# Kernel tuning notes

Measured on AMD Instinct MI355X. Metric: run time of the kernel, lower is better.

The kernel has to match this reference:

```python
import jax, jax.numpy as jnp
import numpy as np

B = 2
C = 96
NH = 4
HD = C // NH
DEPTH = 2
LAT, LON = 181, 360
WH, WW = 6, 12
N = WH * WW
PT, PBm, PL, PR = 2, 3, 0, 0
H, W = LAT + PT + PBm, LON + PL + PR
SH, SW = WH // 2, WW // 2
NWH, NWW = H // WH, W // WW
NW = NWH * NWW
SCALE = HD ** -0.5

def _rel_index():
    ch, cw = np.meshgrid(np.arange(WH), np.arange(WW), indexing='ij')
    coords = np.stack([ch, cw]).reshape(2, -1)
    rel = (coords[:, :, None] - coords[:, None, :]).transpose(1, 2, 0).astype(np.int64)
    rel[:, :, 0] += WH - 1
    rel[:, :, 1] += WW - 1
    rel[:, :, 0] *= 2 * WW - 1
    return rel.sum(-1)  # (N, N)

REL_IDX = jnp.asarray(_rel_index())

def _shift_mask():
    img = np.zeros((H, W))
    cnt = 0
    for hs in (slice(0, -WH), slice(-WH, -SH), slice(-SH, None)):
        for ws in (slice(0, -WW), slice(-WW, -SW), slice(-SW, None)):
            img[hs, ws] = cnt
            cnt += 1
    mw = img.reshape(NWH, WH, NWW, WW).transpose(0, 2, 1, 3).reshape(NW, N)
    am = mw[:, None, :] - mw[:, :, None]
    return np.where(am != 0, -100.0, 0.0).astype(np.float32)

ATTN_MASK = jnp.asarray(_shift_mask())  # (NW, N, N)

def _ln(x, g, b):
    m = x.mean(-1, keepdims=True)
    v = x.var(-1, keepdims=True)
    return (x - m) * jax.lax.rsqrt(v + 1e-5) * g + b

def _win_part(x):
    b = x.shape[0]
    return x.reshape(b, NWH, WH, NWW, WW, C).transpose(0, 1, 3, 2, 4, 5).reshape(-1, N, C)

def _win_rev(xw, b):
    return xw.reshape(b, NWH, NWW, WH, WW, C).transpose(0, 1, 3, 2, 4, 5).reshape(b, H, W, C)

def _block(x, shift, g1, b1, qw, qb, pw, pb, rpb, g2, b2, f1w, f1b, f2w, f2b):
    b = x.shape[0]
    sc = x
    x = _ln(x, g1, b1)
    if shift:
        x = jnp.roll(x, (-SH, -SW), (1, 2))
    xw = _win_part(x)  # (b*NW, N, C)
    qkv = (xw @ qw.T + qb).reshape(-1, N, 3, NH, HD).transpose(2, 0, 3, 1, 4)
    q, k, v = qkv[0], qkv[1], qkv[2]  # each (b*NW, NH, N, HD)
    attn = (q * SCALE) @ k.transpose(0, 1, 3, 2)  # (b*NW, NH, N, N)
    bias = rpb[REL_IDX].transpose(2, 0, 1)  # (NH, N, N)
    attn = attn + bias[None]
    if shift:
        attn = (attn.reshape(b, NW, NH, N, N) + ATTN_MASK[None, :, None]).reshape(-1, NH, N, N)
    attn = jax.nn.softmax(attn, axis=-1)
    out = (attn @ v).transpose(0, 2, 1, 3).reshape(-1, N, C)
    out = out @ pw.T + pb
    x = _win_rev(out, b)
    if shift:
        x = jnp.roll(x, (SH, SW), (1, 2))
    x = sc + x
    h = _ln(x, g2, b2)
    h = jax.nn.gelu(h @ f1w.T + f1b) @ f2w.T + f2b
    return x + h

def _forward(x, g1, b1, qkv_w, qkv_b, proj_w, proj_b, rpb, g2, b2, fc1_w, fc1_b, fc2_w, fc2_b):
    x = jnp.pad(x, ((0, 0), (0, 0), (PT, PBm), (PL, PR)))  # ZeroPad2d
    x = x.transpose(0, 2, 3, 1)  # (B, H, W, C)
    for i in range(DEPTH):
        x = _block(x, i % 2 == 1, g1[i], b1[i], qkv_w[i], qkv_b[i], proj_w[i], proj_b[i],
                   rpb[i], g2[i], b2[i], fc1_w[i], fc1_b[i], fc2_w[i], fc2_b[i])
    x = x.transpose(0, 3, 1, 2)
    return x[:, :, PT:H - PBm, PL:W - PR]


def setup_inputs() -> dict:
    key = jax.random.key(0)
    ks = jax.random.split(key, 6)
    s = 0.02
    tbl = (2 * WH - 1) * (2 * WW - 1)
    return {
        'x': jax.random.normal(ks[0], (B, C, LAT, LON), jnp.float32),
        'g1': jnp.ones((DEPTH, C), jnp.float32),
        'b1': jnp.zeros((DEPTH, C), jnp.float32),
        'qkv_w': jax.random.normal(ks[1], (DEPTH, 3 * C, C), jnp.float32) * s,
        'qkv_b': jnp.zeros((DEPTH, 3 * C), jnp.float32),
        'proj_w': jax.random.normal(ks[2], (DEPTH, C, C), jnp.float32) * s,
        'proj_b': jnp.zeros((DEPTH, C), jnp.float32),
        'rpb': jax.random.normal(ks[3], (DEPTH, tbl, NH), jnp.float32) * s,
        'g2': jnp.ones((DEPTH, C), jnp.float32),
        'b2': jnp.zeros((DEPTH, C), jnp.float32),
        'fc1_w': jax.random.normal(ks[4], (DEPTH, 4 * C, C), jnp.float32) * s,
        'fc1_b': jnp.zeros((DEPTH, 4 * C), jnp.float32),
        'fc2_w': jax.random.normal(ks[5], (DEPTH, C, 4 * C), jnp.float32) * s,
        'fc2_b': jnp.zeros((DEPTH, C), jnp.float32),
    }


def reference(x, g1, b1, qkv_w, qkv_b, proj_w, proj_b, rpb, g2, b2, fc1_w, fc1_b, fc2_w, fc2_b):
    return _forward(x, g1, b1, qkv_w, qkv_b, proj_w, proj_b, rpb, g2, b2, fc1_w, fc1_b, fc2_w, fc2_b)
```

## Files before the change

kernel.cpp:

```cpp
#include <hip/hip_runtime.h>
#include <math.h>

#define BB    2
#define CC    96
#define NHD   4
#define HDIM  24
#define LAT_  181
#define LON_  360
#define PT_   2
#define HH    186
#define WWID  360
#define WH_   6
#define WW_   12
#define NTOK  72
#define SH_   3
#define SW_   6
#define NWH_  31
#define NWW_  30
#define NWIN  930
#define SCALE_ 0.20412414523193154f

typedef __attribute__((ext_vector_type(8))) short short8v;
typedef __attribute__((ext_vector_type(4))) float f32x4;

__device__ __forceinline__ unsigned short pk_bf16(float x) {
    unsigned u = __float_as_uint(x);
    unsigned r = (u + 0x7fffu + ((u >> 16) & 1u)) >> 16;
    return (unsigned short)r;
}
__device__ __forceinline__ uint2 pk4(float a, float b, float c, float d) {
    uint2 r;
    r.x = (unsigned)pk_bf16(a) | ((unsigned)pk_bf16(b) << 16);
    r.y = (unsigned)pk_bf16(c) | ((unsigned)pk_bf16(d) << 16);
    return r;
}

__global__ __launch_bounds__(256) void k_pad2(const float* __restrict__ in, float* __restrict__ X) {
    int bid = blockIdx.x;
    int ct = bid % 3; bid /= 3;
    int wt = bid % 12; bid /= 12;
    int h = bid % HH; int b = bid / HH;
    int lat = h - PT_;
    int tx = threadIdx.x & 31, ty = threadIdx.x >> 5;
    __shared__ float tile[32][33];
    if (lat >= 0 && lat < LAT_) {
        int w = wt * 32 + tx;
        #pragma unroll
        for (int i = 0; i < 4; ++i) {
            int c = ct * 32 + ty + 8 * i;
            float v = 0.f;
            if (w < WWID) v = in[((long)(b * CC + c)) * (LAT_ * LON_) + lat * LON_ + w];
            tile[ty + 8 * i][tx] = v;
        }
    } else {
        #pragma unroll
        for (int i = 0; i < 4; ++i) tile[ty + 8 * i][tx] = 0.f;
    }
    __syncthreads();
    #pragma unroll
    for (int i = 0; i < 4; ++i) {
        int w = wt * 32 + ty + 8 * i;
        if (w < WWID)
            X[(((long)(b * HH + h)) * WWID + w) * CC + ct * 32 + tx] = tile[tx][ty + 8 * i];
    }
}

__global__ __launch_bounds__(256) void k_crop2(const float* __restrict__ X, float* __restrict__ out) {
    int bid = blockIdx.x;
    int ct = bid % 3; bid /= 3;
    int wt = bid % 12; bid /= 12;
    int lat = bid % LAT_; int b = bid / LAT_;
    int h = lat + PT_;
    int tx = threadIdx.x & 31, ty = threadIdx.x >> 5;
    __shared__ float tile[32][33];
    #pragma unroll
    for (int i = 0; i < 4; ++i) {
        int w = wt * 32 + ty + 8 * i;
        if (w < WWID)
            tile[ty + 8 * i][tx] = X[(((long)(b * HH + h)) * WWID + w) * CC + ct * 32 + tx];
    }
    __syncthreads();
    {
        int w = wt * 32 + tx;
        if (w < WWID) {
            #pragma unroll
            for (int i = 0; i < 4; ++i) {
                int c = ct * 32 + ty + 8 * i;
                out[((long)(b * CC + c)) * (LAT_ * LON_) + lat * LON_ + w] = tile[tx][ty + 8 * i];
            }
        }
    }
}

__global__ void k_wprep(const float* __restrict__ f1w, const float* __restrict__ f2w,
                        const float* __restrict__ qkvw, const float* __restrict__ projw,
                        const float* __restrict__ rpb,
                        unsigned short* __restrict__ wbf, float* __restrict__ biasg) {
    int id = blockIdx.x * 256 + threadIdx.x;
    if (id < 73728) {
        int layer = id / 36864, rem = id % 36864;
        int ks = rem / 12288, r2 = rem % 12288;
        int nt = r2 / 512, r3 = r2 % 512;
        int lane = r3 / 8, e = r3 % 8;
        int o = nt * 16 + (lane & 15);
        int c = ks * 32 + 8 * (lane >> 4) + e;
        wbf[(long)layer * 36864 + rem] = pk_bf16(f1w[((long)layer * 384 + o) * 96 + c]);
    } else if (id < 147456) {
        int id2 = id - 73728;
        int layer = id2 / 36864, rem = id2 % 36864;
        int ks = rem / 3072, r2 = rem % 3072;
        int nt = r2 / 512, r3 = r2 % 512;
        int lane = r3 / 8, e = r3 % 8;
        int o = nt * 16 + (lane & 15);
        int c = ks * 32 + 8 * (lane >> 4) + e;
        wbf[73728 + (long)layer * 36864 + rem] = pk_bf16(f2w[((long)layer * 96 + o) * 384 + c]);
    } else if (id < 202752) {
        wbf[id] = pk_bf16(qkvw[id - 147456]);
    } else if (id < 221184) {
        wbf[id] = pk_bf16(projw[id - 202752]);
    } else {
        int id2 = id - 221184;
        int layer = id2 / 102400, r = id2 % 102400;
        int type = r / 25600; r %= 25600;
        int h = r / 6400; r %= 6400;
        int i = r / 80, j = r % 80;
        float v;
        if (i >= 72 || j >= 72) {
            v = -10000.f;
        } else {
            int thi = i / 12, twi = i % 12, thj = j / 12, twj = j % 12;
            int ridx = (thi - thj + 5) * 23 + (twi - twj + 11);
            v = rpb[(layer * 253 + ridx) * 4 + h];
            if (layer == 1) {
                int eh = type & 1, ew = type >> 1;
                int ri = (eh ? (thi < 3 ? 1 : 2) * 3 : 0) + (ew ? (twi < 6 ? 1 : 2) : 0);
                int rj = (eh ? (thj < 3 ? 1 : 2) * 3 : 0) + (ew ? (twj < 6 ? 1 : 2) : 0);
                if (ri != rj) v -= 100.f;
            }
        }
        biasg[id2] = v;
    }
}

template <int SHIFT>
__global__ __launch_bounds__(1024, 4) void k_attn(float* __restrict__ X,
        const float* __restrict__ gg, const float* __restrict__ bb,
        const unsigned short* __restrict__ wqkv, const float* __restrict__ qkvb,
        const unsigned short* __restrict__ wprj, const float* __restrict__ projb,
        const float* __restrict__ biasT) {
    __shared__ __align__(16) unsigned char smem[125184];
    unsigned short* As  = (unsigned short*)smem;
    unsigned short* ps  = (unsigned short*)smem;
    unsigned short* qs  = (unsigned short*)(smem + 66560);
    unsigned short* os  = (unsigned short*)(smem + 66560);
    unsigned short* ks  = (unsigned short*)(smem + 83200);
    unsigned short* vt  = (unsigned short*)(smem + 98560);

    int bid = blockIdx.x;
    int b = bid / NWIN, wi = bid % NWIN;
    int nwh = wi / NWW_, nww = wi % NWW_;
    int tid = threadIdx.x;
    int wv = tid >> 6, lane = tid & 63;
    int li = lane & 15, gq = lane >> 4;

    int type = SHIFT ? ((nwh == 30 ? 1 : 0) | (nww == 29 ? 2 : 0)) : 0;
    const float* bias_t = biasT + type * 25600;

    {
        unsigned* vz = (unsigned*)vt;
        for (int idx = tid; idx < 6656; idx += 1024) vz[idx] = 0u;
        unsigned* az = (unsigned*)(As + 72 * 104);
        for (int idx = tid; idx < 416; idx += 1024) az[idx] = 0u;
    }

    {
        int sub = lane >> 3, p = lane & 7;
        int t = wv * 8 + sub;
        if (t < 72) {
            int th = t / 12, tw = t % 12;
            int hr = nwh * WH_ + th, wr = nww * WW_ + tw;
            int ho = SHIFT ? (hr + SH_) % HH : hr;
            int wo = SHIFT ? (wr + SW_) % WWID : wr;
            const float* xr = X + (((long)b * HH + ho) * WWID + wo) * CC;
            float4 a  = *(const float4*)(xr + p * 4);
            float4 c4 = *(const float4*)(xr + p * 4 + 32);
            float4 e4 = *(const float4*)(xr + p * 4 + 64);
            float s  = a.x + a.y + a.z + a.w + c4.x + c4.y + c4.z + c4.w + e4.x + e4.y + e4.z + e4.w;
            float sq = a.x*a.x + a.y*a.y + a.z*a.z + a.w*a.w + c4.x*c4.x + c4.y*c4.y + c4.z*c4.z + c4.w*c4.w
                     + e4.x*e4.x + e4.y*e4.y + e4.z*e4.z + e4.w*e4.w;
            #pragma unroll
            for (int off = 1; off < 8; off <<= 1) {
                s  += __shfl_xor(s, off);
                sq += __shfl_xor(sq, off);
            }
            float mean = s * (1.f / CC);
            float var = sq * (1.f / CC) - mean * mean;
            float rs = rsqrtf(var + 1e-5f);
            float4 g0 = *(const float4*)(gg + p * 4);
            float4 g1v = *(const float4*)(gg + p * 4 + 32);
            float4 g2v = *(const float4*)(gg + p * 4 + 64);
            float4 t0 = *(const float4*)(bb + p * 4);
            float4 t1 = *(const float4*)(bb + p * 4 + 32);
            float4 t2 = *(const float4*)(bb + p * 4 + 64);
            *(uint2*)(As + t * 104 + p * 4) =
                pk4((a.x - mean) * rs * g0.x + t0.x, (a.y - mean) * rs * g0.y + t0.y,
                    (a.z - mean) * rs * g0.z + t0.z, (a.w - mean) * rs * g0.w + t0.w);
            *(uint2*)(As + t * 104 + p * 4 + 32) =
                pk4((c4.x - mean) * rs * g1v.x + t1.x, (c4.y - mean) * rs * g1v.y + t1.y,
                    (c4.z - mean) * rs * g1v.z + t1.z, (c4.w - mean) * rs * g1v.w + t1.w);
            *(uint2*)(As + t * 104 + p * 4 + 64) =
                pk4((e4.x - mean) * rs * g2v.x + t2.x, (e4.y - mean) * rs * g2v.y + t2.y,
                    (e4.z - mean) * rs * g2v.z + t2.z, (e4.w - mean) * rs * g2v.w + t2.w);
        }
    }
    __syncthreads();

    for (int mt = wv; mt < 18; mt += 16) {
        short8v aw[3];
        #pragma unroll
        for (int ksi = 0; ksi < 3; ++ksi)
            aw[ksi] = *(const short8v*)(wqkv + (mt * 16 + li) * 96 + ksi * 32 + 8 * gq);
        float bias4[4];
        #pragma unroll
        for (int r = 0; r < 4; ++r) bias4[r] = qkvb[mt * 16 + 4 * gq + r];
        f32x4 acc[5];
        #pragma unroll
        for (int nt = 0; nt < 5; ++nt) acc[nt] = (f32x4){0.f, 0.f, 0.f, 0.f};
        #pragma unroll
        for (int nt = 0; nt < 5; ++nt)
            #pragma unroll
            for (int ksi = 0; ksi < 3; ++ksi) {
                short8v by = *(const short8v*)(As + (nt * 16 + li) * 104 + ksi * 32 + 8 * gq);
                acc[nt] = __builtin_amdgcn_mfma_f32_16x16x32_bf16(aw[ksi], by, acc[nt], 0, 0, 0);
            }
        int which = mt / 6, mtl = mt % 6;
        int oo0 = mtl * 16 + 4 * gq;
        int h = oo0 / 24, d0 = oo0 % 24;
        #pragma unroll
        for (int nt = 0; nt < 5; ++nt) {
            int token = nt * 16 + li;
            if (which == 2) {
                #pragma unroll
                for (int r = 0; r < 4; ++r)
                    vt[(h * 32 + d0 + r) * 104 + token] = pk_bf16(acc[nt][r] + bias4[r]);
            } else {
                float v0 = acc[nt][0] + bias4[0], v1 = acc[nt][1] + bias4[1];
                float v2 = acc[nt][2] + bias4[2], v3 = acc[nt][3] + bias4[3];
                if (which == 0) { v0 *= SCALE_; v1 *= SCALE_; v2 *= SCALE_; v3 *= SCALE_; }
                unsigned short* dst = (which == 0 ? qs : ks) + (h * 80 + token) * 24 + d0;
                *(uint2*)dst = pk4(v0, v1, v2, v3);
            }
        }
    }
    __syncthreads();

    for (int u = wv; u < 20; u += 16) {
        int h = u / 5, nt = u % 5;
        int i = nt * 16 + li;
        *(uint2*)(ps + (h * 80 + i) * 104 + 80 + 4 * gq) = (uint2){0u, 0u};
        short8v bq = {0,0,0,0,0,0,0,0};
        if (gq < 3) bq = *(const short8v*)(qs + (h * 80 + i) * 24 + 8 * gq);
        const float* brow = bias_t + (h * 80 + i) * 80;
        float p[20];
        float sum = 0.f;
        #pragma unroll
        for (int mt = 0; mt < 5; ++mt) {
            short8v ak = {0,0,0,0,0,0,0,0};
            if (gq < 3) ak = *(const short8v*)(ks + (h * 80 + mt * 16 + li) * 24 + 8 * gq);
            f32x4 ct = __builtin_amdgcn_mfma_f32_16x16x32_bf16(ak, bq, (f32x4){0.f,0.f,0.f,0.f}, 0, 0, 0);
            float4 bv = *(const float4*)(brow + mt * 16 + 4 * gq);
            p[mt*4+0] = __expf(ct[0] + bv.x);
            p[mt*4+1] = __expf(ct[1] + bv.y);
            p[mt*4+2] = __expf(ct[2] + bv.z);
            p[mt*4+3] = __expf(ct[3] + bv.w);
            sum += p[mt*4+0] + p[mt*4+1] + p[mt*4+2] + p[mt*4+3];
        }
        sum += __shfl_xor(sum, 16);
        sum += __shfl_xor(sum, 32);
        float inv = sum > 0.f ? 1.f / sum : 0.f;
        #pragma unroll
        for (int mt = 0; mt < 5; ++mt)
            *(uint2*)(ps + (h * 80 + i) * 104 + mt * 16 + 4 * gq) =
                pk4(p[mt*4+0] * inv, p[mt*4+1] * inv, p[mt*4+2] * inv, p[mt*4+3] * inv);
    }
    __syncthreads();

    for (int u = wv; u < 40; u += 16) {
        int h = u / 10, rm = u % 10, mt = rm >> 1, nt2 = rm & 1;
        f32x4 acc = (f32x4){0.f, 0.f, 0.f, 0.f};
        #pragma unroll
        for (int ksi = 0; ksi < 3; ++ksi) {
            short8v ap = *(const short8v*)(ps + (h * 80 + mt * 16 + li) * 104 + ksi * 32 + 8 * gq);
            short8v bv = *(const short8v*)(vt + (h * 32 + nt2 * 16 + li) * 104 + ksi * 32 + 8 * gq);
            acc = __builtin_amdgcn_mfma_f32_16x16x32_bf16(ap, bv, acc, 0, 0, 0);
        }
        int d = nt2 * 16 + li;
        if (d < 24) {
            #pragma unroll
            for (int r = 0; r < 4; ++r)
                os[(mt * 16 + 4 * gq + r) * 104 + h * 24 + d] = pk_bf16(acc[r]);
        }
    }
    __syncthreads();

    for (int u = wv; u < 30; u += 16) {
        int mt = u / 6, nt = u % 6;
        f32x4 acc = (f32x4){0.f, 0.f, 0.f, 0.f};
        #pragma unroll
        for (int ksi = 0; ksi < 3; ++ksi) {
            short8v ao = *(const short8v*)(os + (mt * 16 + li) * 104 + ksi * 32 + 8 * gq);
            short8v bw = *(const short8v*)(wprj + (nt * 16 + li) * 96 + ksi * 32 + 8 * gq);
            acc = __builtin_amdgcn_mfma_f32_16x16x32_bf16(ao, bw, acc, 0, 0, 0);
        }
        int o = nt * 16 + li;
        float bo = projb[o];
        #pragma unroll
        for (int r = 0; r < 4; ++r) {
            int token = mt * 16 + 4 * gq + r;
            if (token < 72) {
                int th = token / 12, tw = token % 12;
                int hr = nwh * WH_ + th, wr = nww * WW_ + tw;
                int ho = SHIFT ? (hr + SH_) % HH : hr;
                int wo = SHIFT ? (wr + SW_) % WWID : wr;
                X[(((long)b * HH + ho) * WWID + wo) * CC + o] += acc[r] + bo;
            }
        }
    }
}

__global__ __launch_bounds__(256, 4) void k_mlp_mfma(float* __restrict__ X,
        const float* __restrict__ g, const float* __restrict__ bta,
        const unsigned short* __restrict__ w1f, const float* __restrict__ b1v,
        const unsigned short* __restrict__ w2f, const float* __restrict__ b2v) {
    __shared__ __align__(16) unsigned short As[32 * 120];
    __shared__ __align__(16) unsigned short Hs[32 * 392];
    long tok0 = (long)blockIdx.x * 32;
    int tid = threadIdx.x;

    {
        int t = tid >> 3, p = tid & 7;
        const float* xr = X + (tok0 + t) * CC;
        float4 a = *(const float4*)(xr + p * 4);
        float4 b = *(const float4*)(xr + p * 4 + 32);
        float4 c4 = *(const float4*)(xr + p * 4 + 64);
        float s  = a.x + a.y + a.z + a.w + b.x + b.y + b.z + b.w + c4.x + c4.y + c4.z + c4.w;
        float sq = a.x*a.x + a.y*a.y + a.z*a.z + a.w*a.w + b.x*b.x + b.y*b.y + b.z*b.z + b.w*b.w
                 + c4.x*c4.x + c4.y*c4.y + c4.z*c4.z + c4.w*c4.w;
        #pragma unroll
        for (int off = 1; off < 8; off <<= 1) {
            s  += __shfl_xor(s, off);
            sq += __shfl_xor(sq, off);
        }
        float mean = s * (1.f / CC);
        float var = sq * (1.f / CC) - mean * mean;
        float rs = rsqrtf(var + 1e-5f);
        float4 g0 = *(const float4*)(g + p * 4);
        float4 g1 = *(const float4*)(g + p * 4 + 32);
        float4 g2 = *(const float4*)(g + p * 4 + 64);
        float4 t0 = *(const float4*)(bta + p * 4);
        float4 t1 = *(const float4*)(bta + p * 4 + 32);
        float4 t2 = *(const float4*)(bta + p * 4 + 64);
        unsigned short* arow = As + t * 120;
        arow[p*4+0]  = pk_bf16((a.x - mean) * rs * g0.x + t0.x);
        arow[p*4+1]  = pk_bf16((a.y - mean) * rs * g0.y + t0.y);
        arow[p*4+2]  = pk_bf16((a.z - mean) * rs * g0.z + t0.z);
        arow[p*4+3]  = pk_bf16((a.w - mean) * rs * g0.w + t0.w);
        arow[p*4+32] = pk_bf16((b.x - mean) * rs * g1.x + t1.x);
        arow[p*4+33] = pk_bf16((b.y - mean) * rs * g1.y + t1.y);
        arow[p*4+34] = pk_bf16((b.z - mean) * rs * g1.z + t1.z);
        arow[p*4+35] = pk_bf16((b.w - mean) * rs * g1.w + t1.w);
        arow[p*4+64] = pk_bf16((c4.x - mean) * rs * g2.x + t2.x);
        arow[p*4+65] = pk_bf16((c4.y - mean) * rs * g2.y + t2.y);
        arow[p*4+66] = pk_bf16((c4.z - mean) * rs * g2.z + t2.z);
        arow[p*4+67] = pk_bf16((c4.w - mean) * rs * g2.w + t2.w);
    }
    __syncthreads();

    int w = tid >> 6, lane = tid & 63;
    int wm = w & 1;
    int row = wm * 16 + (lane & 15);
    int kbase = 8 * (lane >> 4);

    {
        int wnh = w >> 1;
        short8v afr[3];
        #pragma unroll
        for (int ks = 0; ks < 3; ++ks)
            afr[ks] = *(const short8v*)(As + row * 120 + ks * 32 + kbase);
        f32x4 acc[12];
        #pragma unroll
        for (int j = 0; j < 12; ++j) acc[j] = (f32x4){0.f, 0.f, 0.f, 0.f};
        const short8v* wb = (const short8v*)w1f;
        #pragma unroll
        for (int j = 0; j < 12; ++j) {
            int nt = wnh * 12 + j;
            #pragma unroll
            for (int ks = 0; ks < 3; ++ks) {
                short8v bfr = wb[(ks * 24 + nt) * 64 + lane];
                acc[j] = __builtin_amdgcn_mfma_f32_16x16x32_bf16(afr[ks], bfr, acc[j], 0, 0, 0);
            }
        }
        #pragma unroll
        for (int j = 0; j < 12; ++j) {
            int n = (wnh * 12 + j) * 16 + (lane & 15);
            float bb = b1v[n];
            #pragma unroll
            for (int r = 0; r < 4; ++r) {
                float s = acc[j][r] + bb;
                float z = s + 0.044715f * s * s * s;
                float gl = s / (1.f + __expf(-1.5957691216057308f * z));
                Hs[(wm * 16 + 4 * (lane >> 4) + r) * 392 + n] = pk_bf16(gl);
            }
        }
    }
    __syncthreads();

    {
        int wnt0 = (w >> 1) * 3;
        f32x4 acc2[3];
        #pragma unroll
        for (int j = 0; j < 3; ++j) acc2[j] = (f32x4){0.f, 0.f, 0.f, 0.f};
        const short8v* wb2 = (const short8v*)w2f;
        #pragma unroll
        for (int ks = 0; ks < 12; ++ks) {
            short8v a2 = *(const short8v*)(Hs + row * 392 + ks * 32 + kbase);
            #pragma unroll
            for (int j = 0; j < 3; ++j) {
                short8v bfr = wb2[(ks * 6 + wnt0 + j) * 64 + lane];
                acc2[j] = __builtin_amdgcn_mfma_f32_16x16x32_bf16(a2, bfr, acc2[j], 0, 0, 0);
            }
        }
        #pragma unroll
        for (int j = 0; j < 3; ++j) {
            int n = (wnt0 + j) * 16 + (lane & 15);
            float bb = b2v[n];
            #pragma unroll
            for (int r = 0; r < 4; ++r) {
                long tok = tok0 + wm * 16 + 4 * (lane >> 4) + r;
                X[tok * CC + n] += acc2[j][r] + bb;
            }
        }
    }
}

extern "C" void kernel_launch(void* const* d_in, const int* in_sizes, int n_in,
                              void* d_out, int out_size, void* d_ws, size_t ws_size,
                              hipStream_t stream) {
    const float* x     = (const float*)d_in[0];
    const float* g1    = (const float*)d_in[1];
    const float* b1    = (const float*)d_in[2];
    const float* qkvw  = (const float*)d_in[3];
    const float* qkvb  = (const float*)d_in[4];
    const float* projw = (const float*)d_in[5];
    const float* projb = (const float*)d_in[6];
    const float* rpb   = (const float*)d_in[7];
    const float* g2    = (const float*)d_in[8];
    const float* b2    = (const float*)d_in[9];
    const float* f1w   = (const float*)d_in[10];
    const float* f1b   = (const float*)d_in[11];
    const float* f2w   = (const float*)d_in[12];
    const float* f2b   = (const float*)d_in[13];

    float* X = (float*)d_ws;
    unsigned short* wbf = (unsigned short*)(X + (long)BB * HH * WWID * CC);
    float* biasg = (float*)(wbf + 221184);

    const int ntok = BB * HH * WWID;

    k_pad2<<<BB * HH * 12 * 3, 256, 0, stream>>>(x, X);
    k_wprep<<<1664, 256, 0, stream>>>(f1w, f2w, qkvw, projw, rpb, wbf, biasg);

    for (int i = 0; i < 2; ++i) {
        const unsigned short* wqkv_bf = wbf + 147456 + (long)i * 27648;
        const unsigned short* wprj_bf = wbf + 202752 + (long)i * 9216;
        if (i == 0) {
            k_attn<0><<<BB * NWIN, 1024, 0, stream>>>(X, g1, b1,
                wqkv_bf, qkvb, wprj_bf, projb, biasg);
        } else {
            k_attn<1><<<BB * NWIN, 1024, 0, stream>>>(X, g1 + CC, b1 + CC,
                wqkv_bf, qkvb + 3 * CC, wprj_bf, projb + CC, biasg + 102400);
        }
        k_mlp_mfma<<<ntok / 32, 256, 0, stream>>>(X,
            g2 + i * CC, b2 + i * CC,
            wbf + (long)i * 36864, f1b + i * 4 * CC,
            wbf + 73728 + (long)i * 36864, f2b + i * CC);
    }

    k_crop2<<<BB * LAT_ * 12 * 3, 256, 0, stream>>>(X, (float*)d_out);
}
```

Before: 346.4 us.

## Fuse softmax and PV per-wave with private P buffers; use native bf16 conversion

The attention kernel now keeps each wave's 16-row softmax probability tile in a private shared-memory slice and runs the P·V MFMAs immediately, dropping one block-wide barrier and the full P matrix in shared memory. The shared-memory layout is rearranged so that os no longer aliases qs, which grows the allocation slightly. The float-to-bf16 packing now uses HIP's intrinsic conversions and packed two-wide conversions, and the layernorm output stores are vectorized to 8-byte writes. The larger shared footprint could affect occupancy.

Measured after the change: 326.7 us. 1.06x faster.

```diff
diff --git a/kernel.cpp b/kernel.cpp
--- a/kernel.cpp
+++ b/kernel.cpp
@@ -1,4 +1,5 @@
 #include <hip/hip_runtime.h>
+#include <hip/hip_bf16.h>
 #include <math.h>
 
 #define BB    2
@@ -24,15 +25,14 @@
 typedef __attribute__((ext_vector_type(4))) float f32x4;
 
 __device__ __forceinline__ unsigned short pk_bf16(float x) {
-    unsigned u = __float_as_uint(x);
-    unsigned r = (u + 0x7fffu + ((u >> 16) & 1u)) >> 16;
-    return (unsigned short)r;
+    __hip_bfloat16 h = __float2bfloat16(x);
+    union { __hip_bfloat16 b; unsigned short u; } cv; cv.b = h; return cv.u;
 }
 __device__ __forceinline__ uint2 pk4(float a, float b, float c, float d) {
-    uint2 r;
-    r.x = (unsigned)pk_bf16(a) | ((unsigned)pk_bf16(b) << 16);
-    r.y = (unsigned)pk_bf16(c) | ((unsigned)pk_bf16(d) << 16);
-    return r;
+    __hip_bfloat162 lo = __float22bfloat162_rn(make_float2(a, b));
+    __hip_bfloat162 hi = __float22bfloat162_rn(make_float2(c, d));
+    union { __hip_bfloat162 b; unsigned u; } c0, c1; c0.b = lo; c1.b = hi;
+    uint2 r; r.x = c0.u; r.y = c1.u; return r;
 }
 
 __global__ __launch_bounds__(256) void k_pad2(const float* __restrict__ in, float* __restrict__ X) {
@@ -148,13 +148,13 @@
         const unsigned short* __restrict__ wqkv, const float* __restrict__ qkvb,
         const unsigned short* __restrict__ wprj, const float* __restrict__ projb,
         const float* __restrict__ biasT) {
-    __shared__ __align__(16) unsigned char smem[125184];
+    __shared__ __align__(16) unsigned char smem[127232];
     unsigned short* As  = (unsigned short*)smem;
-    unsigned short* ps  = (unsigned short*)smem;
-    unsigned short* qs  = (unsigned short*)(smem + 66560);
-    unsigned short* os  = (unsigned short*)(smem + 66560);
-    unsigned short* ks  = (unsigned short*)(smem + 83200);
-    unsigned short* vt  = (unsigned short*)(smem + 98560);
+    unsigned short* psw0= (unsigned short*)smem;
+    unsigned short* qs  = (unsigned short*)(smem + 53248);
+    unsigned short* ks  = (unsigned short*)(smem + 68608);
+    unsigned short* vt  = (unsigned short*)(smem + 83968);
+    unsigned short* os  = (unsigned short*)(smem + 110592);
 
     int bid = blockIdx.x;
     int b = bid / NWIN, wi = bid % NWIN;
@@ -256,11 +256,11 @@
 
     for (int u = wv; u < 20; u += 16) {
         int h = u / 5, nt = u % 5;
-        int i = nt * 16 + li;
-        *(uint2*)(ps + (h * 80 + i) * 104 + 80 + 4 * gq) = (uint2){0u, 0u};
+        unsigned short* psw = psw0 + (size_t)wv * (16 * 104);
+        *(uint2*)(psw + li * 104 + 80 + 4 * gq) = (uint2){0u, 0u};
         short8v bq = {0,0,0,0,0,0,0,0};
-        if (gq < 3) bq = *(const short8v*)(qs + (h * 80 + i) * 24 + 8 * gq);
-        const float* brow = bias_t + (h * 80 + i) * 80;
+        if (gq < 3) bq = *(const short8v*)(qs + (h * 80 + nt * 16 + li) * 24 + 8 * gq);
+        const float* brow = bias_t + (h * 80 + nt * 16 + li) * 80;
         float p[20];
         float sum = 0.f;
         #pragma unroll
@@ -280,25 +280,23 @@
         float inv = sum > 0.f ? 1.f / sum : 0.f;
         #pragma unroll
         for (int mt = 0; mt < 5; ++mt)
-            *(uint2*)(ps + (h * 80 + i) * 104 + mt * 16 + 4 * gq) =
+            *(uint2*)(psw + li * 104 + mt * 16 + 4 * gq) =
                 pk4(p[mt*4+0] * inv, p[mt*4+1] * inv, p[mt*4+2] * inv, p[mt*4+3] * inv);
-    }
-    __syncthreads();
-
-    for (int u = wv; u < 40; u += 16) {
-        int h = u / 10, rm = u % 10, mt = rm >> 1, nt2 = rm & 1;
-        f32x4 acc = (f32x4){0.f, 0.f, 0.f, 0.f};
-        #pragma unroll
-        for (int ksi = 0; ksi < 3; ++ksi) {
-            short8v ap = *(const short8v*)(ps + (h * 80 + mt * 16 + li) * 104 + ksi * 32 + 8 * gq);
-            short8v bv = *(const short8v*)(vt + (h * 32 + nt2 * 16 + li) * 104 + ksi * 32 + 8 * gq);
-            acc = __builtin_amdgcn_mfma_f32_16x16x32_bf16(ap, bv, acc, 0, 0, 0);
-        }
-        int d = nt2 * 16 + li;
-        if (d < 24) {
-            #pragma unroll
-            for (int r = 0; r < 4; ++r)
-                os[(mt * 16 + 4 * gq + r) * 104 + h * 24 + d] = pk_bf16(acc[r]);
+        #pragma unroll
+        for (int nt2 = 0; nt2 < 2; ++nt2) {
+            f32x4 acc = (f32x4){0.f, 0.f, 0.f, 0.f};
+            #pragma unroll
+            for (int ksi = 0; ksi < 3; ++ksi) {
+                short8v ap = *(const short8v*)(psw + li * 104 + ksi * 32 + 8 * gq);
+                short8v bv = *(const short8v*)(vt + (h * 32 + nt2 * 16 + li) * 104 + ksi * 32 + 8 * gq);
+                acc = __builtin_amdgcn_mfma_f32_16x16x32_bf16(ap, bv, acc, 0, 0, 0);
+            }
+            int d = nt2 * 16 + li;
+            if (d < 24) {
+                #pragma unroll
+                for (int r = 0; r < 4; ++r)
+                    os[(nt * 16 + 4 * gq + r) * 104 + h * 24 + d] = pk_bf16(acc[r]);
+            }
         }
     }
     __syncthreads();
@@ -361,18 +359,15 @@
         float4 t1 = *(const float4*)(bta + p * 4 + 32);
         float4 t2 = *(const float4*)(bta + p * 4 + 64);
         unsigned short* arow = As + t * 120;
-        arow[p*4+0]  = pk_bf16((a.x - mean) * rs * g0.x + t0.x);
-        arow[p*4+1]  = pk_bf16((a.y - mean) * rs * g0.y + t0.y);
-        arow[p*4+2]  = pk_bf16((a.z - mean) * rs * g0.z + t0.z);
-        arow[p*4+3]  = pk_bf16((a.w - mean) * rs * g0.w + t0.w);
-        arow[p*4+32] = pk_bf16((b.x - mean) * rs * g1.x + t1.x);
-        arow[p*4+33] = pk_bf16((b.y - mean) * rs * g1.y + t1.y);
-        arow[p*4+34] = pk_bf16((b.z - mean) * rs * g1.z + t1.z);
-        arow[p*4+35] = pk_bf16((b.w - mean) * rs * g1.w + t1.w);
-        arow[p*4+64] = pk_bf16((c4.x - mean) * rs * g2.x + t2.x);
-        arow[p*4+65] = pk_bf16((c4.y - mean) * rs * g2.y + t2.y);
-        arow[p*4+66] = pk_bf16((c4.z - mean) * rs * g2.z + t2.z);
-        arow[p*4+67] = pk_bf16((c4.w - mean) * rs * g2.w + t2.w);
+        *(uint2*)(arow + p * 4) =
+            pk4((a.x - mean) * rs * g0.x + t0.x, (a.y - mean) * rs * g0.y + t0.y,
+                (a.z - mean) * rs * g0.z + t0.z, (a.w - mean) * rs * g0.w + t0.w);
+        *(uint2*)(arow + p * 4 + 32) =
+            pk4((b.x - mean) * rs * g1.x + t1.x, (b.y - mean) * rs * g1.y + t1.y,
+                (b.z - mean) * rs * g1.z + t1.z, (b.w - mean) * rs * g1.w + t1.w);
+        *(uint2*)(arow + p * 4 + 64) =
+            pk4((c4.x - mean) * rs * g2.x + t2.x, (c4.y - mean) * rs * g2.y + t2.y,
+                (c4.z - mean) * rs * g2.z + t2.z, (c4.w - mean) * rs * g2.w + t2.w);
     }
     __syncthreads();
 
```
